# Optimization experiments

Measured on AMD Instinct MI355X. Metric: run time of the kernel, lower is better.

The kernel has to match this reference:

```python
import jax, jax.numpy as jnp
import numpy as np

E = 8        # num experts
TOP = 2      # top-k
D = 1024     # emb_size


def setup_inputs() -> dict:
    key = jax.random.key(0)
    ks = jax.random.split(key, 8)
    s = 1.0 / np.sqrt(D)
    x = jax.random.normal(ks[0], (4, 2048, D), dtype=jnp.float32)
    Wg = jax.random.uniform(ks[1], (D, E), jnp.float32, -s, s)
    bg = jax.random.uniform(ks[2], (E,), jnp.float32, -s, s)
    W1 = jax.random.uniform(ks[3], (E, D, D), jnp.float32, -s, s)
    b1 = jax.random.uniform(ks[4], (E, D), jnp.float32, -s, s)
    W2 = jax.random.uniform(ks[5], (E, D, D), jnp.float32, -s, s)
    b2 = jax.random.uniform(ks[6], (E, D), jnp.float32, -s, s)
    return {"x": x, "Wg": Wg, "bg": bg, "W1": W1, "b1": b1, "W2": W2, "b2": b2}


def reference(x, Wg, bg, W1, b1, W2, b2):
    x_shape = x.shape
    xt = x.reshape(-1, x_shape[-1])                       # [N, D] tokens
    gate_prob = jax.nn.softmax(xt @ Wg + bg, axis=-1)     # [N, E]
    top_w, top_i = jax.lax.top_k(gate_prob, TOP)          # [N, TOP]
    top_w = jax.nn.softmax(top_w, axis=-1)                # renormalize over top-k
    N = xt.shape[0]
    # combine weights scattered into dense [N, E] (each token has TOP nonzeros)
    comb = jnp.zeros((N, E), xt.dtype).at[jnp.arange(N)[:, None], top_i].add(top_w)
    # per-expert 2-layer MLP applied to all tokens; masked-out tokens get 0 combine weight
    h = jax.nn.relu(jnp.einsum('nd,edf->enf', xt, W1) + b1[:, None, :])   # [E, N, D]
    ye = jnp.einsum('enf,efg->eng', h, W2) + b2[:, None, :]               # [E, N, D]
    y = jnp.einsum('ne,eng->ng', comb, ye)                                # [N, D]
    return y.reshape(x_shape), gate_prob
```

## Files before the change

### kernel.cpp

```cpp
#include <hip/hip_runtime.h>
#include <stdint.h>

#define TOKENS 8192
#define DIM    1024
#define NEXP   8
#define NASSIGN (TOKENS*2)

#define C_ROW   16
#define C_TILE  25
#define C_TOTAL 34

#define WS_CTRL  0
#define WS_TOPE  1024
#define WS_TOPW  (WS_TOPE + NASSIGN*4)
#define WS_PTOK  (WS_TOPW + NASSIGN*4)
#define WS_AROW  (WS_PTOK + NASSIGN*4)
#define WS_XB    (WS_AROW + NASSIGN*4)
#define WS_W1T   (WS_XB  + (size_t)TOKENS*DIM*2)
#define WS_W2T   (WS_W1T + (size_t)NEXP*DIM*DIM*2)
#define WS_H     (WS_W2T + (size_t)NEXP*DIM*DIM*2)
#define WS_YE    WS_XB

#define WGLD (DIM + 4)

typedef __attribute__((ext_vector_type(8))) short short8;
typedef __attribute__((ext_vector_type(4))) float floatx4;

__device__ __forceinline__ uint32_t bfr(float f) {
  uint32_t v = __float_as_uint(f);
  return (v + 0x7FFFu + ((v >> 16) & 1u)) >> 16;
}
__device__ __forceinline__ float b2f(uint32_t u) { return __uint_as_float(u << 16); }

__device__ __forceinline__ void load_lds16(const void* g, void* l) {
  __builtin_amdgcn_global_load_lds(
      (const __attribute__((address_space(1))) uint32_t*)g,
      (__attribute__((address_space(3))) uint32_t*)l, 16, 0, 0);
}

__global__ __launch_bounds__(256) void gateconv_kernel(
    const float* __restrict__ x, const float* __restrict__ Wg,
    const float* __restrict__ bg, float* __restrict__ gate_out,
    int* __restrict__ top_e, float* __restrict__ top_w,
    uint16_t* __restrict__ xb) {
  __shared__ float wgs[NEXP * WGLD];
  int t = threadIdx.x;
  #pragma unroll
  for (int k = 0; k < 32; k++) {
    int i = k * 256 + t;
    float v = Wg[i];
    wgs[(i & 7) * WGLD + (i >> 3)] = v;
  }
  __syncthreads();

  int wave = t >> 6, lane = t & 63;
  int tok = blockIdx.x * 4 + wave;
  const float4* xr = (const float4*)(x + (size_t)tok * DIM);
  uint2* xw = (uint2*)(xb + (size_t)tok * DIM);

  float4 acc[NEXP];
  #pragma unroll
  for (int e = 0; e < NEXP; e++) acc[e] = make_float4(0.f, 0.f, 0.f, 0.f);

  #pragma unroll
  for (int c = 0; c < 4; c++) {
    float4 xv = xr[c * 64 + lane];
    uint2 o;
    o.x = bfr(xv.x) | (bfr(xv.y) << 16);
    o.y = bfr(xv.z) | (bfr(xv.w) << 16);
    xw[c * 64 + lane] = o;
    int d0 = (c * 64 + lane) * 4;
    #pragma unroll
    for (int e = 0; e < NEXP; e++) {
      float4 wv = *(const float4*)&wgs[e * WGLD + d0];
      acc[e].x = fmaf(xv.x, wv.x, acc[e].x);
      acc[e].y = fmaf(xv.y, wv.y, acc[e].y);
      acc[e].z = fmaf(xv.z, wv.z, acc[e].z);
      acc[e].w = fmaf(xv.w, wv.w, acc[e].w);
    }
  }
  float s[NEXP];
  #pragma unroll
  for (int e = 0; e < NEXP; e++) s[e] = (acc[e].x + acc[e].y) + (acc[e].z + acc[e].w);
  #pragma unroll
  for (int off = 32; off > 0; off >>= 1) {
    #pragma unroll
    for (int e = 0; e < NEXP; e++) s[e] += __shfl_xor(s[e], off);
  }
  if (lane == 0) {
    float lg[NEXP], p[NEXP];
    float mx = -1e30f;
    #pragma unroll
    for (int e = 0; e < NEXP; e++) { lg[e] = s[e] + bg[e]; mx = fmaxf(mx, lg[e]); }
    float sum = 0.f;
    #pragma unroll
    for (int e = 0; e < NEXP; e++) { p[e] = expf(lg[e] - mx); sum += p[e]; }
    float inv = 1.f / sum;
    #pragma unroll
    for (int e = 0; e < NEXP; e++) p[e] *= inv;
    float4* go = (float4*)(gate_out + (size_t)tok * NEXP);
    go[0] = make_float4(p[0], p[1], p[2], p[3]);
    go[1] = make_float4(p[4], p[5], p[6], p[7]);
    int i1 = 0;
    #pragma unroll
    for (int e = 1; e < NEXP; e++) if (p[e] > p[i1]) i1 = e;
    int i2 = (i1 == 0) ? 1 : 0;
    #pragma unroll
    for (int e = 0; e < NEXP; e++) if (e != i1 && p[e] > p[i2]) i2 = e;
    float ev = expf(p[i2] - p[i1]);
    float w1 = 1.f / (1.f + ev), w2 = ev / (1.f + ev);
    top_e[2*tok]   = i1; top_e[2*tok+1] = i2;
    top_w[2*tok]   = w1; top_w[2*tok+1] = w2;
  }
}

__global__ void convw_kernel(const float* __restrict__ W1, const float* __restrict__ W2,
                             uint16_t* __restrict__ W1T, uint16_t* __restrict__ W2T) {
  __shared__ uint16_t tile[64][65];
  int m = blockIdx.z;
  const float* src = (m < 8) ? (W1 + (size_t)m*DIM*DIM) : (W2 + (size_t)(m-8)*DIM*DIM);
  uint16_t*    dst = (m < 8) ? (W1T + (size_t)m*DIM*DIM) : (W2T + (size_t)(m-8)*DIM*DIM);
  int d0 = blockIdx.y * 64, f0 = blockIdx.x * 64;
  int t = threadIdx.x;
  int col = t & 63, rb = (t >> 6) * 16;
  #pragma unroll
  for (int i = 0; i < 16; i++) {
    int dr = rb + i;
    tile[dr][col] = (uint16_t)bfr(src[(size_t)(d0+dr)*DIM + f0 + col]);
  }
  __syncthreads();
  #pragma unroll
  for (int i = 0; i < 16; i++) {
    int fr = rb + i;
    dst[(size_t)(f0+fr)*DIM + d0 + col] = tile[col][fr];
  }
}

__global__ __launch_bounds__(1024) void route_kernel(
    const int* __restrict__ top_e, int* __restrict__ ctrl,
    int* __restrict__ ptok, int* __restrict__ arow) {
  __shared__ int sc[NEXP * 1024];
  __shared__ int scnt[NEXP];
  __shared__ int rowstart[NEXP];
  int t = threadIdx.x;
  int e_loc[16];
  int cnt[NEXP];
  #pragma unroll
  for (int e = 0; e < NEXP; e++) cnt[e] = 0;
  #pragma unroll
  for (int j = 0; j < 16; j++) {
    int e = top_e[t * 16 + j];
    e_loc[j] = e;
    cnt[e]++;
  }
  #pragma unroll
  for (int e = 0; e < NEXP; e++) sc[e * 1024 + t] = cnt[e];
  __syncthreads();
  int wave = t >> 6, lane = t & 63;
  if (wave < NEXP) {
    int running = 0;
    for (int chunk = 0; chunk < 16; chunk++) {
      int idx = wave * 1024 + chunk * 64 + lane;
      int v = sc[idx];
      int incl = v;
      #pragma unroll
      for (int off = 1; off < 64; off <<= 1) {
        int u = __shfl_up(incl, off);
        if (lane >= off) incl += u;
      }
      sc[idx] = running + incl - v;
      running += __shfl(incl, 63);
    }
    if (lane == 0) scnt[wave] = running;
  }
  __syncthreads();
  if (t == 0) {
    int rs = 0, ts = 0;
    for (int e = 0; e < NEXP; e++) {
      ctrl[C_ROW + e] = rs;
      ctrl[C_TILE + e] = ts;
      rowstart[e] = rs;
      int c = scnt[e];
      rs += c;
      ts += (c + 127) >> 7;
    }
    ctrl[C_ROW + NEXP] = rs;
    ctrl[C_TILE + NEXP] = ts;
    ctrl[C_TOTAL] = ts;
  }
  __syncthreads();
  int off[NEXP];
  #pragma unroll
  for (int e = 0; e < NEXP; e++) off[e] = rowstart[e] + sc[e * 1024 + t];
  #pragma unroll
  for (int j = 0; j < 16; j++) {
    int i = t * 16 + j;
    int e = e_loc[j];
    int pos = off[e]++;
    ptok[pos] = i >> 1;
    arow[i] = pos;
  }
}

__global__ __launch_bounds__(256, 2) void gemm1_kernel(
    const uint16_t* __restrict__ xb, const uint16_t* __restrict__ w1t,
    const float* __restrict__ b1, const int* __restrict__ ctrl,
    const int* __restrict__ ptok, uint16_t* __restrict__ h) {
  __shared__ __align__(16) uint16_t As[128*32];
  __shared__ __align__(16) uint16_t Bs[128*32];
  int mtile = blockIdx.x;
  if (mtile >= ctrl[C_TOTAL]) return;
  int e = 0;
  #pragma unroll
  for (int k = 1; k < NEXP; k++) if (mtile >= ctrl[C_TILE + k]) e = k;
  int row0 = ctrl[C_ROW + e] + (mtile - ctrl[C_TILE + e]) * 128;
  int rend = ctrl[C_ROW + e + 1];
  int n0 = blockIdx.y * 128;

  int t = threadIdx.x, lane = t & 63, w = t >> 6;
  const uint16_t* gA[2];
  const uint16_t* gB[2];
  #pragma unroll
  for (int i = 0; i < 2; i++) {
    int c = w*128 + i*64 + lane;
    int row = c >> 2, kc = c & 3;
    int ar = row0 + row; if (ar > NASSIGN-1) ar = NASSIGN-1;
    int tok = ptok[ar];
    gA[i] = xb  + (size_t)tok * DIM + kc*8;
    gB[i] = w1t + (size_t)e*DIM*DIM + (size_t)(n0 + row)*DIM + kc*8;
  }
  floatx4 acc[4][4];
  #pragma unroll
  for (int mi = 0; mi < 4; mi++)
    #pragma unroll
    for (int ni = 0; ni < 4; ni++) acc[mi][ni] = (floatx4)(0.f);

  int wm = w & 1, wn = w >> 1;
  int l15 = lane & 15, lq = lane >> 4;

  for (int kt = 0; kt < DIM/32; kt++) {
    #pragma unroll
    for (int i = 0; i < 2; i++) {
      load_lds16(gA[i], &As[(w*128 + i*64) * 8]);
      load_lds16(gB[i], &Bs[(w*128 + i*64) * 8]);
      gA[i] += 32; gB[i] += 32;
    }
    __syncthreads();
    short8 a[4], b[4];
    #pragma unroll
    for (int mi = 0; mi < 4; mi++)
      a[mi] = *(const short8*)&As[(wm*64 + mi*16 + l15)*32 + lq*8];
    #pragma unroll
    for (int ni = 0; ni < 4; ni++)
      b[ni] = *(const short8*)&Bs[(wn*64 + ni*16 + l15)*32 + lq*8];
    #pragma unroll
    for (int mi = 0; mi < 4; mi++)
      #pragma unroll
      for (int ni = 0; ni < 4; ni++)
        acc[mi][ni] = __builtin_amdgcn_mfma_f32_16x16x32_bf16(a[mi], b[ni], acc[mi][ni], 0, 0, 0);
    __syncthreads();
  }
  #pragma unroll
  for (int mi = 0; mi < 4; mi++) {
    #pragma unroll
    for (int r = 0; r < 4; r++) {
      int rt = wm*64 + mi*16 + lq*4 + r;
      int ar = row0 + rt;
      if (ar < rend) {
        #pragma unroll
        for (int ni = 0; ni < 4; ni++) {
          int n = n0 + wn*64 + ni*16 + l15;
          float v = acc[mi][ni][r] + b1[e*DIM + n];
          v = fmaxf(v, 0.f);
          h[(size_t)ar*DIM + n] = (uint16_t)bfr(v);
        }
      }
    }
  }
}

__global__ __launch_bounds__(256, 2) void gemm2_kernel(
    const uint16_t* __restrict__ h, const uint16_t* __restrict__ w2t,
    const float* __restrict__ b2, const int* __restrict__ ctrl,
    uint16_t* __restrict__ yeb) {
  __shared__ __align__(16) uint16_t As[128*32];
  __shared__ __align__(16) uint16_t Bs[128*32];
  int mtile = blockIdx.x;
  if (mtile >= ctrl[C_TOTAL]) return;
  int e = 0;
  #pragma unroll
  for (int k = 1; k < NEXP; k++) if (mtile >= ctrl[C_TILE + k]) e = k;
  int row0 = ctrl[C_ROW + e] + (mtile - ctrl[C_TILE + e]) * 128;
  int rend = ctrl[C_ROW + e + 1];
  int n0 = blockIdx.y * 128;

  int t = threadIdx.x, lane = t & 63, w = t >> 6;
  const uint16_t* gA[2];
  const uint16_t* gB[2];
  #pragma unroll
  for (int i = 0; i < 2; i++) {
    int c = w*128 + i*64 + lane;
    int row = c >> 2, kc = c & 3;
    int ar = row0 + row; if (ar > NASSIGN-1) ar = NASSIGN-1;
    gA[i] = h   + (size_t)ar * DIM + kc*8;
    gB[i] = w2t + (size_t)e*DIM*DIM + (size_t)(n0 + row)*DIM + kc*8;
  }
  floatx4 acc[4][4];
  #pragma unroll
  for (int mi = 0; mi < 4; mi++)
    #pragma unroll
    for (int ni = 0; ni < 4; ni++) acc[mi][ni] = (floatx4)(0.f);

  int wm = w & 1, wn = w >> 1;
  int l15 = lane & 15, lq = lane >> 4;

  for (int kt = 0; kt < DIM/32; kt++) {
    #pragma unroll
    for (int i = 0; i < 2; i++) {
      load_lds16(gA[i], &As[(w*128 + i*64) * 8]);
      load_lds16(gB[i], &Bs[(w*128 + i*64) * 8]);
      gA[i] += 32; gB[i] += 32;
    }
    __syncthreads();
    short8 a[4], b[4];
    #pragma unroll
    for (int mi = 0; mi < 4; mi++)
      a[mi] = *(const short8*)&As[(wm*64 + mi*16 + l15)*32 + lq*8];
    #pragma unroll
    for (int ni = 0; ni < 4; ni++)
      b[ni] = *(const short8*)&Bs[(wn*64 + ni*16 + l15)*32 + lq*8];
    #pragma unroll
    for (int mi = 0; mi < 4; mi++)
      #pragma unroll
      for (int ni = 0; ni < 4; ni++)
        acc[mi][ni] = __builtin_amdgcn_mfma_f32_16x16x32_bf16(a[mi], b[ni], acc[mi][ni], 0, 0, 0);
    __syncthreads();
  }
  #pragma unroll
  for (int mi = 0; mi < 4; mi++) {
    #pragma unroll
    for (int r = 0; r < 4; r++) {
      int rt = wm*64 + mi*16 + lq*4 + r;
      int ar = row0 + rt;
      if (ar < rend) {
        #pragma unroll
        for (int ni = 0; ni < 4; ni++) {
          int n = n0 + wn*64 + ni*16 + l15;
          float v = acc[mi][ni][r] + b2[e*DIM + n];
          yeb[(size_t)ar*DIM + n] = (uint16_t)bfr(v);
        }
      }
    }
  }
}

__global__ __launch_bounds__(256) void combine_kernel(
    const uint16_t* __restrict__ yeb, const int* __restrict__ arow,
    const float* __restrict__ top_w, float* __restrict__ y) {
  int tok = blockIdx.x, t = threadIdx.x;
  int r0 = arow[2*tok], r1 = arow[2*tok+1];
  float w0 = top_w[2*tok], w1 = top_w[2*tok+1];
  const uint2* a = (const uint2*)(yeb + (size_t)r0 * DIM);
  const uint2* b = (const uint2*)(yeb + (size_t)r1 * DIM);
  uint2 av = a[t], bv = b[t];
  float4 o;
  o.x = w0 * b2f(av.x & 0xFFFFu) + w1 * b2f(bv.x & 0xFFFFu);
  o.y = w0 * b2f(av.x >> 16)     + w1 * b2f(bv.x >> 16);
  o.z = w0 * b2f(av.y & 0xFFFFu) + w1 * b2f(bv.y & 0xFFFFu);
  o.w = w0 * b2f(av.y >> 16)     + w1 * b2f(bv.y >> 16);
  ((float4*)(y + (size_t)tok * DIM))[t] = o;
}

extern "C" void kernel_launch(void* const* d_in, const int* in_sizes, int n_in,
                              void* d_out, int out_size, void* d_ws, size_t ws_size,
                              hipStream_t stream) {
  const float* x  = (const float*)d_in[0];
  const float* Wg = (const float*)d_in[1];
  const float* bg = (const float*)d_in[2];
  const float* W1 = (const float*)d_in[3];
  const float* b1 = (const float*)d_in[4];
  const float* W2 = (const float*)d_in[5];
  const float* b2 = (const float*)d_in[6];
  float* out = (float*)d_out;
  char* ws = (char*)d_ws;

  int*      ctrl = (int*)(ws + WS_CTRL);
  int*      tope = (int*)(ws + WS_TOPE);
  float*    topw = (float*)(ws + WS_TOPW);
  int*      ptok = (int*)(ws + WS_PTOK);
  int*      arow = (int*)(ws + WS_AROW);
  uint16_t* xb   = (uint16_t*)(ws + WS_XB);
  uint16_t* w1t  = (uint16_t*)(ws + WS_W1T);
  uint16_t* w2t  = (uint16_t*)(ws + WS_W2T);
  uint16_t* hbuf = (uint16_t*)(ws + WS_H);
  uint16_t* yeb  = (uint16_t*)(ws + WS_YE);

  convw_kernel<<<dim3(16,16,16), 256, 0, stream>>>(W1, W2, w1t, w2t);
  gateconv_kernel<<<2048, 256, 0, stream>>>(x, Wg, bg, out + (size_t)TOKENS*DIM,
                                            tope, topw, xb);
  route_kernel<<<1, 1024, 0, stream>>>(tope, ctrl, ptok, arow);

  gemm1_kernel<<<dim3(136, 8), 256, 0, stream>>>(xb, w1t, b1, ctrl, ptok, hbuf);
  gemm2_kernel<<<dim3(136, 8), 256, 0, stream>>>(hbuf, w2t, b2, ctrl, yeb);
  combine_kernel<<<TOKENS, 256, 0, stream>>>(yeb, arow, topw, out);
}
```

Baseline: 307.0 us.

## Double GEMM K-tile to 64 with XOR-swizzled LDS, N-fastest block order, vectorized transpose

The expert GEMMs now stage 64-wide K slices instead of 32, which halves the number of barrier pairs per tile. LDS is laid out with an XOR swizzle on 16-byte chunks to avoid bank conflicts on the short8 fragment reads. Launch becomes 1D with the N tile in the low bits, so the 8 N-blocks sharing one A row tile are scheduled next to each other for L2 reuse of the gathered rows. The weight transpose kernel writes 4 bf16 values per store. Doubling the LDS tile raises shared memory per block to 32KB, which may limit occupancy.

```diff
diff --git a/kernel.cpp b/kernel.cpp
--- a/kernel.cpp
+++ b/kernel.cpp
@@ -5,6 +5,7 @@
 #define DIM    1024
 #define NEXP   8
 #define NASSIGN (TOKENS*2)
+#define BK     64
 
 #define C_ROW   16
 #define C_TILE  25
@@ -116,7 +117,7 @@
 
 __global__ void convw_kernel(const float* __restrict__ W1, const float* __restrict__ W2,
                              uint16_t* __restrict__ W1T, uint16_t* __restrict__ W2T) {
-  __shared__ uint16_t tile[64][65];
+  __shared__ uint16_t tile[64][68];
   int m = blockIdx.z;
   const float* src = (m < 8) ? (W1 + (size_t)m*DIM*DIM) : (W2 + (size_t)(m-8)*DIM*DIM);
   uint16_t*    dst = (m < 8) ? (W1T + (size_t)m*DIM*DIM) : (W2T + (size_t)(m-8)*DIM*DIM);
@@ -129,10 +130,16 @@
     tile[dr][col] = (uint16_t)bfr(src[(size_t)(d0+dr)*DIM + f0 + col]);
   }
   __syncthreads();
-  #pragma unroll
-  for (int i = 0; i < 16; i++) {
-    int fr = rb + i;
-    dst[(size_t)(f0+fr)*DIM + d0 + col] = tile[col][fr];
+  int dg = t & 15, frb = t >> 4;
+  #pragma unroll
+  for (int i = 0; i < 4; i++) {
+    int fr = frb + i * 16;
+    uint32_t b0 = tile[dg*4+0][fr], b1 = tile[dg*4+1][fr];
+    uint32_t b2 = tile[dg*4+2][fr], b3 = tile[dg*4+3][fr];
+    uint2 v;
+    v.x = b0 | (b1 << 16);
+    v.y = b2 | (b3 << 16);
+    *(uint2*)&dst[(size_t)(f0+fr)*DIM + d0 + dg*4] = v;
   }
 }
 
@@ -206,28 +213,29 @@
     const uint16_t* __restrict__ xb, const uint16_t* __restrict__ w1t,
     const float* __restrict__ b1, const int* __restrict__ ctrl,
     const int* __restrict__ ptok, uint16_t* __restrict__ h) {
-  __shared__ __align__(16) uint16_t As[128*32];
-  __shared__ __align__(16) uint16_t Bs[128*32];
-  int mtile = blockIdx.x;
+  __shared__ __align__(16) uint16_t As[128*BK];
+  __shared__ __align__(16) uint16_t Bs[128*BK];
+  int mtile = blockIdx.x >> 3;
   if (mtile >= ctrl[C_TOTAL]) return;
+  int n0 = (blockIdx.x & 7) * 128;
   int e = 0;
   #pragma unroll
   for (int k = 1; k < NEXP; k++) if (mtile >= ctrl[C_TILE + k]) e = k;
   int row0 = ctrl[C_ROW + e] + (mtile - ctrl[C_TILE + e]) * 128;
   int rend = ctrl[C_ROW + e + 1];
-  int n0 = blockIdx.y * 128;
 
   int t = threadIdx.x, lane = t & 63, w = t >> 6;
-  const uint16_t* gA[2];
-  const uint16_t* gB[2];
-  #pragma unroll
-  for (int i = 0; i < 2; i++) {
-    int c = w*128 + i*64 + lane;
-    int row = c >> 2, kc = c & 3;
+  const uint16_t* gA[4];
+  const uint16_t* gB[4];
+  #pragma unroll
+  for (int i = 0; i < 4; i++) {
+    int s = i * 256 + t;
+    int row = s >> 3, cs = s & 7;
+    int gc = cs ^ (row & 7);
     int ar = row0 + row; if (ar > NASSIGN-1) ar = NASSIGN-1;
     int tok = ptok[ar];
-    gA[i] = xb  + (size_t)tok * DIM + kc*8;
-    gB[i] = w1t + (size_t)e*DIM*DIM + (size_t)(n0 + row)*DIM + kc*8;
+    gA[i] = xb  + (size_t)tok * DIM + gc*8;
+    gB[i] = w1t + (size_t)e*DIM*DIM + (size_t)(n0 + row)*DIM + gc*8;
   }
   floatx4 acc[4][4];
   #pragma unroll
@@ -238,26 +246,35 @@
   int wm = w & 1, wn = w >> 1;
   int l15 = lane & 15, lq = lane >> 4;
 
-  for (int kt = 0; kt < DIM/32; kt++) {
-    #pragma unroll
-    for (int i = 0; i < 2; i++) {
-      load_lds16(gA[i], &As[(w*128 + i*64) * 8]);
-      load_lds16(gB[i], &Bs[(w*128 + i*64) * 8]);
-      gA[i] += 32; gB[i] += 32;
+  for (int kt = 0; kt < DIM/BK; kt++) {
+    #pragma unroll
+    for (int i = 0; i < 4; i++) {
+      load_lds16(gA[i], &As[(i*256 + t) * 8]);
+      load_lds16(gB[i], &Bs[(i*256 + t) * 8]);
+      gA[i] += BK; gB[i] += BK;
     }
     __syncthreads();
-    short8 a[4], b[4];
-    #pragma unroll
-    for (int mi = 0; mi < 4; mi++)
-      a[mi] = *(const short8*)&As[(wm*64 + mi*16 + l15)*32 + lq*8];
-    #pragma unroll
-    for (int ni = 0; ni < 4; ni++)
-      b[ni] = *(const short8*)&Bs[(wn*64 + ni*16 + l15)*32 + lq*8];
-    #pragma unroll
-    for (int mi = 0; mi < 4; mi++)
-      #pragma unroll
-      for (int ni = 0; ni < 4; ni++)
-        acc[mi][ni] = __builtin_amdgcn_mfma_f32_16x16x32_bf16(a[mi], b[ni], acc[mi][ni], 0, 0, 0);
+    #pragma unroll
+    for (int ks = 0; ks < 2; ks++) {
+      short8 a[4], b[4];
+      #pragma unroll
+      for (int mi = 0; mi < 4; mi++) {
+        int row = wm*64 + mi*16 + l15;
+        int slot = (ks*4 + lq) ^ (row & 7);
+        a[mi] = *(const short8*)&As[row*BK + slot*8];
+      }
+      #pragma unroll
+      for (int ni = 0; ni < 4; ni++) {
+        int row = wn*64 + ni*16 + l15;
+        int slot = (ks*4 + lq) ^ (row & 7);
+        b[ni] = *(const short8*)&Bs[row*BK + slot*8];
+      }
+      #pragma unroll
+      for (int mi = 0; mi < 4; mi++)
+        #pragma unroll
+        for (int ni = 0; ni < 4; ni++)
+          acc[mi][ni] = __builtin_amdgcn_mfma_f32_16x16x32_bf16(a[mi], b[ni], acc[mi][ni], 0, 0, 0);
+    }
     __syncthreads();
   }
   #pragma unroll
@@ -283,27 +300,28 @@
     const uint16_t* __restrict__ h, const uint16_t* __restrict__ w2t,
     const float* __restrict__ b2, const int* __restrict__ ctrl,
     uint16_t* __restrict__ yeb) {
-  __shared__ __align__(16) uint16_t As[128*32];
-  __shared__ __align__(16) uint16_t Bs[128*32];
-  int mtile = blockIdx.x;
+  __shared__ __align__(16) uint16_t As[128*BK];
+  __shared__ __align__(16) uint16_t Bs[128*BK];
+  int mtile = blockIdx.x >> 3;
   if (mtile >= ctrl[C_TOTAL]) return;
+  int n0 = (blockIdx.x & 7) * 128;
   int e = 0;
   #pragma unroll
   for (int k = 1; k < NEXP; k++) if (mtile >= ctrl[C_TILE + k]) e = k;
   int row0 = ctrl[C_ROW + e] + (mtile - ctrl[C_TILE + e]) * 128;
   int rend = ctrl[C_ROW + e + 1];
-  int n0 = blockIdx.y * 128;
 
   int t = threadIdx.x, lane = t & 63, w = t >> 6;
-  const uint16_t* gA[2];
-  const uint16_t* gB[2];
-  #pragma unroll
-  for (int i = 0; i < 2; i++) {
-    int c = w*128 + i*64 + lane;
-    int row = c >> 2, kc = c & 3;
+  const uint16_t* gA[4];
+  const uint16_t* gB[4];
+  #pragma unroll
+  for (int i = 0; i < 4; i++) {
+    int s = i * 256 + t;
+    int row = s >> 3, cs = s & 7;
+    int gc = cs ^ (row & 7);
     int ar = row0 + row; if (ar > NASSIGN-1) ar = NASSIGN-1;
-    gA[i] = h   + (size_t)ar * DIM + kc*8;
-    gB[i] = w2t + (size_t)e*DIM*DIM + (size_t)(n0 + row)*DIM + kc*8;
+    gA[i] = h   + (size_t)ar * DIM + gc*8;
+    gB[i] = w2t + (size_t)e*DIM*DIM + (size_t)(n0 + row)*DIM + gc*8;
   }
   floatx4 acc[4][4];
   #pragma unroll
@@ -314,26 +332,35 @@
   int wm = w & 1, wn = w >> 1;
   int l15 = lane & 15, lq = lane >> 4;
 
-  for (int kt = 0; kt < DIM/32; kt++) {
-    #pragma unroll
-    for (int i = 0; i < 2; i++) {
-      load_lds16(gA[i], &As[(w*128 + i*64) * 8]);
-      load_lds16(gB[i], &Bs[(w*128 + i*64) * 8]);
-      gA[i] += 32; gB[i] += 32;
+  for (int kt = 0; kt < DIM/BK; kt++) {
+    #pragma unroll
+    for (int i = 0; i < 4; i++) {
+      load_lds16(gA[i], &As[(i*256 + t) * 8]);
+      load_lds16(gB[i], &Bs[(i*256 + t) * 8]);
+      gA[i] += BK; gB[i] += BK;
     }
     __syncthreads();
-    short8 a[4], b[4];
-    #pragma unroll
-    for (int mi = 0; mi < 4; mi++)
-      a[mi] = *(const short8*)&As[(wm*64 + mi*16 + l15)*32 + lq*8];
-    #pragma unroll
-    for (int ni = 0; ni < 4; ni++)
-      b[ni] = *(const short8*)&Bs[(wn*64 + ni*16 + l15)*32 + lq*8];
-    #pragma unroll
-    for (int mi = 0; mi < 4; mi++)
-      #pragma unroll
-      for (int ni = 0; ni < 4; ni++)
-        acc[mi][ni] = __builtin_amdgcn_mfma_f32_16x16x32_bf16(a[mi], b[ni], acc[mi][ni], 0, 0, 0);
+    #pragma unroll
+    for (int ks = 0; ks < 2; ks++) {
+      short8 a[4], b[4];
+      #pragma unroll
+      for (int mi = 0; mi < 4; mi++) {
+        int row = wm*64 + mi*16 + l15;
+        int slot = (ks*4 + lq) ^ (row & 7);
+        a[mi] = *(const short8*)&As[row*BK + slot*8];
+      }
+      #pragma unroll
+      for (int ni = 0; ni < 4; ni++) {
+        int row = wn*64 + ni*16 + l15;
+        int slot = (ks*4 + lq) ^ (row & 7);
+        b[ni] = *(const short8*)&Bs[row*BK + slot*8];
+      }
+      #pragma unroll
+      for (int mi = 0; mi < 4; mi++)
+        #pragma unroll
+        for (int ni = 0; ni < 4; ni++)
+          acc[mi][ni] = __builtin_amdgcn_mfma_f32_16x16x32_bf16(a[mi], b[ni], acc[mi][ni], 0, 0, 0);
+    }
     __syncthreads();
   }
   #pragma unroll
@@ -400,7 +427,7 @@
                                             tope, topw, xb);
   route_kernel<<<1, 1024, 0, stream>>>(tope, ctrl, ptok, arow);
 
-  gemm1_kernel<<<dim3(136, 8), 256, 0, stream>>>(xb, w1t, b1, ctrl, ptok, hbuf);
-  gemm2_kernel<<<dim3(136, 8), 256, 0, stream>>>(hbuf, w2t, b2, ctrl, yeb);
+  gemm1_kernel<<<136*8, 256, 0, stream>>>(xb, w1t, b1, ctrl, ptok, hbuf);
+  gemm2_kernel<<<136*8, 256, 0, stream>>>(hbuf, w2t, b2, ctrl, yeb);
   combine_kernel<<<TOKENS, 256, 0, stream>>>(yeb, arow, topw, out);
 }
```

Measured after the change: 293.5 us. -4.4%, faster.
